# Kernel optimization log

Measured on AMD Instinct MI355X. Metric: run time of the kernel, lower is better.

Reference implementation:

```python
import jax, jax.numpy as jnp
from jax import lax
import numpy as np

SOBEL_X = jnp.array([[-1., 0., 1.], [-2., 0., 2.], [-1., 0., 1.]], dtype=jnp.float32)
SOBEL_Y = jnp.array([[-1., -2., -1.], [0., 0., 0.], [1., 2., 1.]], dtype=jnp.float32)
ALIVE_CH = 3
ALIVE_TH = 0.1
DROPOUT = 0.0
CLAMP = 5.0


def _dwconv3(x, k):
    """Depthwise 3x3 conv, padding=1 (SAME). x: [B,C,H,W], k: [3,3]."""
    C = x.shape[1]
    kern = jnp.tile(k[None, None], (C, 1, 1, 1))  # [C,1,3,3] OIHW, groups=C
    return lax.conv_general_dilated(
        x, kern, window_strides=(1, 1), padding='SAME',
        feature_group_count=C, dimension_numbers=('NCHW', 'OIHW', 'NCHW'))


def _maxpool3(a):
    """3x3 max pool, stride 1, padding 1. a: [B,1,H,W]."""
    return lax.reduce_window(a, -jnp.inf, lax.max, (1, 1, 3, 3), (1, 1, 1, 1), 'SAME')


def setup_inputs() -> dict:
    key = jax.random.key(0)
    kx, k1, k2 = jax.random.split(key, 3)
    B, C, H, W = 8, 16, 128, 128
    hidden = 128
    x = jax.random.uniform(kx, (B, C, H, W), dtype=jnp.float32)  # alive-ish states
    w1 = jax.random.normal(k1, (hidden, 3 * C), dtype=jnp.float32) * 0.05
    b1 = jnp.zeros((hidden,), dtype=jnp.float32)
    w2 = jax.random.normal(k2, (C, hidden), dtype=jnp.float32) * 0.05
    b2 = jnp.zeros((C,), dtype=jnp.float32)
    return {"x": x, "w1": w1, "b1": b1, "w2": w2, "b2": b2, "num_steps": 8}


def reference(x, w1, b1, w2, b2, num_steps):
    keys = jax.random.split(jax.random.key(42), num_steps)

    def step(s, k):
        # pre-update alive mask: maxpool over alive channel > threshold
        pre = _maxpool3(s[:, ALIVE_CH:ALIVE_CH + 1]) > ALIVE_TH  # [B,1,H,W] bool
        # stochastic update mask (dropout=0 -> effectively all ones)
        upd_mask = (jax.random.uniform(k, s.shape) > DROPOUT).astype(s.dtype)
        # perceive: identity conv (padding=1) == s itself; sobel depthwise convs
        perceived = jnp.concatenate(
            [s, _dwconv3(s, SOBEL_X), _dwconv3(s, SOBEL_Y)], axis=1)  # [B,3C,H,W]
        # pointwise update MLP (1x1 convs)
        h = jax.nn.relu(jnp.einsum('bchw,oc->bohw', perceived, w1)
                        + b1[None, :, None, None])
        dx = jnp.einsum('bchw,oc->bohw', h, w2) + b2[None, :, None, None]
        # residual update with clamp
        dx = jnp.clip(dx, -CLAMP, CLAMP)
        s = s + upd_mask * dx
        # post-update alive mask; keep cells alive both before and after
        post = _maxpool3(s[:, ALIVE_CH:ALIVE_CH + 1]) > ALIVE_TH
        s = s * (pre & post).astype(s.dtype)
        return s, None

    x, _ = lax.scan(step, x, keys)
    return x
```

## Files before the change

### kernel.cpp

```cpp
#include <hip/hip_runtime.h>
#include <stdint.h>


#define BATCH 8
#define CH 16
#define HT 128
#define WD 128
#define HIDN 128
#define PLANE (HT*WD)
#define IMG (CH*PLANE)
#define NELEM (BATCH*IMG)
#define NPIX (BATCH*PLANE)
#define WORDS_PER_STEP (NELEM/32)
#define NSTEPS 8

#define PSTR 72
#define PLO_OFF 2304
#define KCM_OFF 4608
#define KF_OFF  5056
#define WREG    5504

typedef _Float16 f16x8 __attribute__((ext_vector_type(8)));
typedef _Float16 f16x4 __attribute__((ext_vector_type(4)));
typedef float    f32x4 __attribute__((ext_vector_type(4)));

struct Keys { unsigned k[2*NSTEPS]; };

__host__ __device__ __forceinline__ unsigned rotl32u(unsigned v, int r) {
  return (v << r) | (v >> (32 - r));
}

__host__ __device__ __forceinline__ void tf2x32(unsigned k0, unsigned k1,
                                                unsigned c0, unsigned c1,
                                                unsigned &o0, unsigned &o1) {
  const unsigned ks2 = k0 ^ k1 ^ 0x1BD11BDAu;
  unsigned x0 = c0 + k0, x1 = c1 + k1;
  x0 += x1; x1 = rotl32u(x1, 13); x1 ^= x0;
  x0 += x1; x1 = rotl32u(x1, 15); x1 ^= x0;
  x0 += x1; x1 = rotl32u(x1, 26); x1 ^= x0;
  x0 += x1; x1 = rotl32u(x1,  6); x1 ^= x0;
  x0 += k1; x1 += ks2 + 1u;
  x0 += x1; x1 = rotl32u(x1, 17); x1 ^= x0;
  x0 += x1; x1 = rotl32u(x1, 29); x1 ^= x0;
  x0 += x1; x1 = rotl32u(x1, 16); x1 ^= x0;
  x0 += x1; x1 = rotl32u(x1, 24); x1 ^= x0;
  x0 += ks2; x1 += k0 + 2u;
  x0 += x1; x1 = rotl32u(x1, 13); x1 ^= x0;
  x0 += x1; x1 = rotl32u(x1, 15); x1 ^= x0;
  x0 += x1; x1 = rotl32u(x1, 26); x1 ^= x0;
  x0 += x1; x1 = rotl32u(x1,  6); x1 ^= x0;
  x0 += k0; x1 += k1 + 3u;
  x0 += x1; x1 = rotl32u(x1, 17); x1 ^= x0;
  x0 += x1; x1 = rotl32u(x1, 29); x1 ^= x0;
  x0 += x1; x1 = rotl32u(x1, 16); x1 ^= x0;
  x0 += x1; x1 = rotl32u(x1, 24); x1 ^= x0;
  x0 += k1; x1 += ks2 + 4u;
  x0 += x1; x1 = rotl32u(x1, 13); x1 ^= x0;
  x0 += x1; x1 = rotl32u(x1, 15); x1 ^= x0;
  x0 += x1; x1 = rotl32u(x1, 26); x1 ^= x0;
  x0 += x1; x1 = rotl32u(x1,  6); x1 ^= x0;
  x0 += ks2; x1 += k0 + 5u;
  o0 = x0; o1 = x1;
}

__global__ __launch_bounds__(256) void mask_kernel(unsigned* __restrict__ mask,
                                                   Keys keys) {
  unsigned t = blockIdx.x * 256u + threadIdx.x;
  unsigned step = t >> 16;
  unsigned k0 = keys.k[2*step], k1 = keys.k[2*step + 1];
  unsigned base = (t & 65535u) << 5;
  unsigned word = 0u;
  #pragma unroll 4
  for (int i = 0; i < 32; ++i) {
    unsigned b1x, b2x;
    tf2x32(k0, k1, 0u, base + (unsigned)i, b1x, b2x);
    unsigned bits = b1x ^ b2x;
    word |= (((bits >> 9) != 0u) ? 1u : 0u) << i;
  }
  mask[t] = word;
}

__global__ __launch_bounds__(256) void wpack_kernel(
    const float* __restrict__ w1, const float* __restrict__ w2,
    _Float16* __restrict__ w1fh, _Float16* __restrict__ w1fl,
    _Float16* __restrict__ w2fh, _Float16* __restrict__ w2fl) {
  int t = blockIdx.x * 256 + threadIdx.x;
  if (t < 8192) {
    int lane = (t >> 3) & 63, i = t & 7;
    int kt = t >> 12, nt = (t >> 9) & 7;
    int k = kt * 32 + (lane >> 4) * 8 + i;
    int n = nt * 16 + (lane & 15);
    float v = (k < 48) ? w1[n * 48 + k] : 0.f;
    _Float16 h = (_Float16)v;
    w1fh[t] = h;
    w1fl[t] = (_Float16)(v - (float)h);
  } else {
    int u = t - 8192;
    int lane = (u >> 3) & 63, i = u & 7;
    int kt = u >> 9;
    int g = (lane >> 4) & 3;
    int o = lane & 15;
    int kk = (i < 4) ? (4 * g + i) : (16 + 4 * g + (i - 4));
    float v = w2[o * HIDN + kt * 32 + kk];
    _Float16 h = (_Float16)v;
    w2fh[u] = h;
    w2fl[u] = (_Float16)(v - (float)h);
  }
}

__global__ __launch_bounds__(256, 3) void step_mfma(
    const float* __restrict__ s,
    const f16x8* __restrict__ w1fh, const f16x8* __restrict__ w1fl,
    const f16x8* __restrict__ w2fh, const f16x8* __restrict__ w2fl,
    const float* __restrict__ bias1, const float* __restrict__ bias2,
    const unsigned* __restrict__ mask,
    float* __restrict__ mid,
    const float* __restrict__ mid3cR,
    float* __restrict__ mid3cW,
    const unsigned char* __restrict__ preR,
    unsigned char* __restrict__ preW,
    const int hasKill) {
  __shared__ __align__(16) char smem[4 * WREG];
  const int tid = threadIdx.x;
  const int wv = tid >> 6;
  const int l  = tid & 63;
  const int p  = l & 15;
  const int g  = l >> 4;
  char* wb = smem + wv * WREG;
  _Float16* Phi = (_Float16*)wb;
  _Float16* Plo = (_Float16*)(wb + PLO_OFF);
  float*    kcm = (float*)(wb + KCM_OFF);
  float*    kfl = (float*)(wb + KF_OFF);

  const int pid0 = blockIdx.x * 128 + wv * 32;
  const int b  = pid0 >> 14;
  const int r0 = pid0 & 16383;
  const int y  = r0 >> 7;
  const int x0 = r0 & 127;
  const bool yu = (y > 0), yd = (y < HT - 1);

  if (hasKill) {
    const float* m3 = mid3cR + b * PLANE;
    #pragma unroll
    for (int rr = 0; rr < 2; ++rr) {
      const int e = l + rr * 64;
      if (e < 108) {
        const int kr = e / 36;
        const int kc = e - kr * 36;
        const int xx = x0 - 2 + kc;
        float cm = -1e30f;
        if ((unsigned)xx < WD) {
          #pragma unroll
          for (int dr = -1; dr <= 1; ++dr) {
            const int ry = y - 1 + kr + dr;
            if ((unsigned)ry < HT) cm = fmaxf(cm, m3[ry * WD + xx]);
          }
        }
        kcm[kr * 36 + kc] = cm;
      }
    }
    asm volatile("" ::: "memory");
    const unsigned char* prb = preR + b * PLANE;
    #pragma unroll
    for (int rr = 0; rr < 2; ++rr) {
      const int e = l + rr * 64;
      if (e < 102) {
        const int kr = e / 34;
        const int kc = e - kr * 34;
        const int yy = y - 1 + kr;
        const int xx = x0 - 1 + kc;
        float kf = 0.f;
        if ((unsigned)yy < HT && (unsigned)xx < WD) {
          const float* c0 = kcm + kr * 36 + kc;
          float mx = fmaxf(fmaxf(c0[0], c0[1]), c0[2]);
          kf = ((mx > 0.1f) && prb[yy * WD + xx]) ? 1.f : 0.f;
        }
        kfl[kr * 36 + kc] = kf;
      }
    }
  } else {
    #pragma unroll
    for (int rr = 0; rr < 2; ++rr) {
      const int e = l + rr * 64;
      if (e < 108) kfl[e] = 1.f;
    }
  }

  const float4 b2q = *(const float4*)(bias2 + g * 4);
  unsigned mw[4];
  #pragma unroll
  for (int cc = 0; cc < 4; ++cc)
    mw[cc] = mask[((b * CH + g * 4 + cc) * HT + y) * (WD / 32) + (x0 >> 5)];

  {
    uint4 z; z.x = 0u; z.y = 0u; z.z = 0u; z.w = 0u;
    _Float16* zb = (l & 32) ? Plo : Phi;
    *(uint4*)(zb + (l & 15) * PSTR + 48 + ((l >> 4) & 1) * 8) = z;
  }

  asm volatile("" ::: "memory");

  const float* sb = s + b * IMG;
  float sctr[2][4];
  float premax[2] = {-1e30f, -1e30f};
  f16x8 pbh[2][2], pbl[2][2];
  #pragma unroll
  for (int t = 0; t < 2; ++t) {
    const int xt = x0 + 16 * t + p;
    const int ctr = y * WD + xt;
    const bool xl = (xt > 0), xr = (xt < WD - 1);
    float kf9[9];
    {
      const int kc = 16 * t + p;
      #pragma unroll
      for (int dy2 = 0; dy2 < 3; ++dy2)
        #pragma unroll
        for (int dx2 = 0; dx2 < 3; ++dx2)
          kf9[dy2 * 3 + dx2] = kfl[dy2 * 36 + kc + dx2];
    }
    f16x4 vh0, vh1, vh2, vl0, vl1, vl2;
    #pragma unroll
    for (int cc = 0; cc < 4; ++cc) {
      const int c = g * 4 + cc;
      const float* sc = sb + c * PLANE + ctr;
      float a11 = sc[0] * kf9[4];
      float a00 = ((yu && xl) ? sc[-WD - 1] : 0.f) * kf9[0];
      float a01 = (yu         ? sc[-WD]     : 0.f) * kf9[1];
      float a02 = ((yu && xr) ? sc[-WD + 1] : 0.f) * kf9[2];
      float a10 = (xl         ? sc[-1]      : 0.f) * kf9[3];
      float a12 = (xr         ? sc[1]       : 0.f) * kf9[5];
      float a20 = ((yd && xl) ? sc[WD - 1]  : 0.f) * kf9[6];
      float a21 = (yd         ? sc[WD]      : 0.f) * kf9[7];
      float a22 = ((yd && xr) ? sc[WD + 1]  : 0.f) * kf9[8];
      float sx = (a02 - a00) + 2.f * (a12 - a10) + (a22 - a20);
      float sy = (a20 - a00) + 2.f * (a21 - a01) + (a22 - a02);
      sctr[t][cc] = a11;
      _Float16 h0 = (_Float16)a11;
      _Float16 h1 = (_Float16)sx;
      _Float16 h2 = (_Float16)sy;
      vh0[cc] = h0; vl0[cc] = (_Float16)(a11 - (float)h0);
      vh1[cc] = h1; vl1[cc] = (_Float16)(sx - (float)h1);
      vh2[cc] = h2; vl2[cc] = (_Float16)(sy - (float)h2);
      if (g == 0 && cc == 3) {
        float m0 = fmaxf(fmaxf(a00, a01), fmaxf(a02, a10));
        float m1 = fmaxf(fmaxf(a11, a12), fmaxf(a20, a21));
        premax[t] = fmaxf(fmaxf(m0, m1), a22);
      }
    }
    *(f16x4*)(Phi + p * PSTR + 4 * g)      = vh0;
    *(f16x4*)(Phi + p * PSTR + 16 + 4 * g) = vh1;
    *(f16x4*)(Phi + p * PSTR + 32 + 4 * g) = vh2;
    *(f16x4*)(Plo + p * PSTR + 4 * g)      = vl0;
    *(f16x4*)(Plo + p * PSTR + 16 + 4 * g) = vl1;
    *(f16x4*)(Plo + p * PSTR + 32 + 4 * g) = vl2;
    asm volatile("" ::: "memory");
    const _Float16* prow = Phi + p * PSTR;
    const _Float16* lrow = Plo + p * PSTR;
    pbh[t][0] = *(const f16x8*)(prow + g * 8);
    pbh[t][1] = *(const f16x8*)(prow + 32 + g * 8);
    pbl[t][0] = *(const f16x8*)(lrow + g * 8);
    pbl[t][1] = *(const f16x8*)(lrow + 32 + g * 8);
    asm volatile("" ::: "memory");
  }

  f32x4 acc[2][8];
  #pragma unroll
  for (int nt = 0; nt < 8; ++nt) {
    const float4 bq = *(const float4*)(bias1 + nt * 16 + 4 * g);
    f32x4 v = {bq.x, bq.y, bq.z, bq.w};
    acc[0][nt] = v;
    acc[1][nt] = v;
  }
  #pragma unroll
  for (int nt = 0; nt < 8; ++nt) {
    f16x8 w1h0 = w1fh[nt * 64 + l];
    f16x8 w1h1 = w1fh[512 + nt * 64 + l];
    f16x8 w1l0 = w1fl[nt * 64 + l];
    f16x8 w1l1 = w1fl[512 + nt * 64 + l];
    #pragma unroll
    for (int t = 0; t < 2; ++t) {
      acc[t][nt] = __builtin_amdgcn_mfma_f32_16x16x32_f16(w1h0, pbh[t][0], acc[t][nt], 0, 0, 0);
      acc[t][nt] = __builtin_amdgcn_mfma_f32_16x16x32_f16(w1h1, pbh[t][1], acc[t][nt], 0, 0, 0);
      acc[t][nt] = __builtin_amdgcn_mfma_f32_16x16x32_f16(w1l0, pbh[t][0], acc[t][nt], 0, 0, 0);
      acc[t][nt] = __builtin_amdgcn_mfma_f32_16x16x32_f16(w1l1, pbh[t][1], acc[t][nt], 0, 0, 0);
      acc[t][nt] = __builtin_amdgcn_mfma_f32_16x16x32_f16(w1h0, pbl[t][0], acc[t][nt], 0, 0, 0);
      acc[t][nt] = __builtin_amdgcn_mfma_f32_16x16x32_f16(w1h1, pbl[t][1], acc[t][nt], 0, 0, 0);
    }
  }

  f16x8 w2h[4], w2l[4];
  #pragma unroll
  for (int kt = 0; kt < 4; ++kt) {
    w2h[kt] = w2fh[kt * 64 + l];
    w2l[kt] = w2fl[kt * 64 + l];
  }

  f32x4 dxr[2];
  #pragma unroll
  for (int t = 0; t < 2; ++t) {
    f16x8 hB[4], lB[4];
    #pragma unroll
    for (int kt = 0; kt < 4; ++kt) {
      #pragma unroll
      for (int i2 = 0; i2 < 4; ++i2) {
        float h0 = fmaxf(acc[t][2 * kt][i2], 0.f);
        _Float16 hh0 = (_Float16)h0;
        hB[kt][i2] = hh0;
        lB[kt][i2] = (_Float16)(h0 - (float)hh0);
        float h1 = fmaxf(acc[t][2 * kt + 1][i2], 0.f);
        _Float16 hh1 = (_Float16)h1;
        hB[kt][4 + i2] = hh1;
        lB[kt][4 + i2] = (_Float16)(h1 - (float)hh1);
      }
    }
    f32x4 accP = {b2q.x, b2q.y, b2q.z, b2q.w};
    f32x4 accQ = {0.f, 0.f, 0.f, 0.f};
    f32x4 accR = {0.f, 0.f, 0.f, 0.f};
    #pragma unroll
    for (int kt = 0; kt < 4; ++kt) {
      accP = __builtin_amdgcn_mfma_f32_16x16x32_f16(w2h[kt], hB[kt], accP, 0, 0, 0);
      accQ = __builtin_amdgcn_mfma_f32_16x16x32_f16(w2l[kt], hB[kt], accQ, 0, 0, 0);
      accR = __builtin_amdgcn_mfma_f32_16x16x32_f16(w2h[kt], lB[kt], accR, 0, 0, 0);
    }
    dxr[t] = (accP + accQ) + accR;
  }

  if (g == 0) {
    preW[pid0 + p]      = (premax[0] > 0.1f) ? 1 : 0;
    preW[pid0 + 16 + p] = (premax[1] > 0.1f) ? 1 : 0;
  }

  #pragma unroll
  for (int t = 0; t < 2; ++t) {
    const int xt = x0 + 16 * t + p;
    const int rt = y * WD + xt;
    #pragma unroll
    for (int cc = 0; cc < 4; ++cc) {
      const int c = g * 4 + cc;
      float d = dxr[t][cc];
      d = fminf(fmaxf(d, -5.f), 5.f);
      float v = sctr[t][cc] + (((mw[cc] >> (16 * t + p)) & 1u) ? d : 0.f);
      mid[b * IMG + c * PLANE + rt] = v;
      if (g == 0 && cc == 3) mid3cW[pid0 + 16 * t + p] = v;
    }
  }
}

__global__ __launch_bounds__(256) void step_b(
    const float* __restrict__ mid,
    const unsigned char* __restrict__ pre,
    float* __restrict__ out) {
  int t = blockIdx.x * 256 + threadIdx.x;
  int cq = t >> 15;
  int qid = t & 32767;
  int b = qid >> 12;
  int r = qid & 4095;
  int y = r >> 5;
  int x0 = (r & 31) * 4;
  const float* m3 = mid + b * IMG + 3 * PLANE;

  float col[6];
  #pragma unroll
  for (int j = 0; j < 6; ++j) {
    int xx = x0 - 1 + j;
    float m = -1e30f;
    if ((unsigned)xx < WD) {
      #pragma unroll
      for (int dy = -1; dy <= 1; ++dy) {
        int yy = y + dy;
        if ((unsigned)yy < HT) m = fmaxf(m, m3[yy * WD + xx]);
      }
    }
    col[j] = m;
  }

  const unsigned char* pr = pre + b * PLANE + y * WD + x0;
  float f[4];
  #pragma unroll
  for (int i = 0; i < 4; ++i) {
    float mx = fmaxf(fmaxf(col[i], col[i + 1]), col[i + 2]);
    f[i] = ((mx > 0.1f) && pr[i]) ? 1.f : 0.f;
  }

  #pragma unroll
  for (int cc = 0; cc < 4; ++cc) {
    int c = cq * 4 + cc;
    const float4 v = *(const float4*)&mid[b * IMG + c * PLANE + y * WD + x0];
    float4 w;
    w.x = v.x * f[0]; w.y = v.y * f[1]; w.z = v.z * f[2]; w.w = v.w * f[3];
    *(float4*)&out[b * IMG + c * PLANE + y * WD + x0] = w;
  }
}

extern "C" void kernel_launch(void* const* d_in, const int* in_sizes, int n_in,
                              void* d_out, int out_size, void* d_ws, size_t ws_size,
                              hipStream_t stream) {
  const float* x  = (const float*)d_in[0];
  const float* w1 = (const float*)d_in[1];
  const float* b1 = (const float*)d_in[2];
  const float* w2 = (const float*)d_in[3];
  const float* b2 = (const float*)d_in[4];
  float* out = (float*)d_out;

  char* ws = (char*)d_ws;
  float* midbuf[2];
  midbuf[0] = (float*)ws;
  midbuf[1] = (float*)(ws + (size_t)NELEM * 4);
  float* m3b[2];
  m3b[0] = (float*)(ws + 2 * (size_t)NELEM * 4);
  m3b[1] = m3b[0] + NPIX;
  unsigned char* preb[2];
  preb[0] = (unsigned char*)(ws + 2 * (size_t)NELEM * 4 + 2 * (size_t)NPIX * 4);
  preb[1] = preb[0] + NPIX;
  unsigned* mask = (unsigned*)(ws + 2 * (size_t)NELEM * 4
                                  + 2 * (size_t)NPIX * 4 + 2 * (size_t)NPIX);
  _Float16* w1fh = (_Float16*)((char*)mask
                               + (size_t)NSTEPS * WORDS_PER_STEP * 4);
  _Float16* w1fl = w1fh + 8192;
  _Float16* w2fh = w1fl + 8192;
  _Float16* w2fl = w2fh + 2048;

  Keys keys;
  for (int j = 0; j < NSTEPS; ++j) {
    unsigned a, b;
    tf2x32(0u, 42u, 0u, (unsigned)j, a, b);
    keys.k[2 * j] = a; keys.k[2 * j + 1] = b;
  }

  mask_kernel<<<(NSTEPS * WORDS_PER_STEP) / 256, 256, 0, stream>>>(mask, keys);
  wpack_kernel<<<40, 256, 0, stream>>>(w1, w2, w1fh, w1fl, w2fh, w2fl);

  for (int s = 0; s < NSTEPS; ++s) {
    const float* src = (s == 0) ? x : midbuf[(s - 1) & 1];
    const int cur = s & 1, prv = cur ^ 1;
    step_mfma<<<NPIX / 128, 256, 0, stream>>>(
        src,
        (const f16x8*)w1fh, (const f16x8*)w1fl,
        (const f16x8*)w2fh, (const f16x8*)w2fl,
        b1, b2, mask + s * WORDS_PER_STEP,
        midbuf[cur],
        m3b[prv], m3b[cur],
        preb[prv], preb[cur],
        (s > 0) ? 1 : 0);
  }
  step_b<<<NPIX / 256, 256, 0, stream>>>(
      midbuf[(NSTEPS - 1) & 1], preb[(NSTEPS - 1) & 1], out);
}
```

Before: 266.8 us.

## Fuse threefry dropout mask generation into step kernel and prefetch stencil taps

Removes the separate mask_kernel, which precomputed dropout bitmasks for all steps, and instead generates each wave's mask words inside step_mfma with threefry, passing the per-step keys as kernel arguments and combining bytes via lane shuffles into shared memory. The 9-tap stencil loads are also hoisted to the start of the kernel, ahead of the alive-mask computation, so global loads overlap with the mask and kill setup. This drops one launch and the mask memory traffic, but adds threefry ALU work and register pressure (72 tap floats per thread) to the main step kernel.

```diff
diff --git a/kernel.cpp b/kernel.cpp
--- a/kernel.cpp
+++ b/kernel.cpp
@@ -11,14 +11,14 @@
 #define IMG (CH*PLANE)
 #define NELEM (BATCH*IMG)
 #define NPIX (BATCH*PLANE)
-#define WORDS_PER_STEP (NELEM/32)
 #define NSTEPS 8
 
 #define PSTR 72
 #define PLO_OFF 2304
 #define KCM_OFF 4608
 #define KF_OFF  5056
-#define WREG    5504
+#define KMW_OFF 5488
+#define WREG    5552
 
 typedef _Float16 f16x8 __attribute__((ext_vector_type(8)));
 typedef _Float16 f16x4 __attribute__((ext_vector_type(4)));
@@ -63,23 +63,6 @@
   o0 = x0; o1 = x1;
 }
 
-__global__ __launch_bounds__(256) void mask_kernel(unsigned* __restrict__ mask,
-                                                   Keys keys) {
-  unsigned t = blockIdx.x * 256u + threadIdx.x;
-  unsigned step = t >> 16;
-  unsigned k0 = keys.k[2*step], k1 = keys.k[2*step + 1];
-  unsigned base = (t & 65535u) << 5;
-  unsigned word = 0u;
-  #pragma unroll 4
-  for (int i = 0; i < 32; ++i) {
-    unsigned b1x, b2x;
-    tf2x32(k0, k1, 0u, base + (unsigned)i, b1x, b2x);
-    unsigned bits = b1x ^ b2x;
-    word |= (((bits >> 9) != 0u) ? 1u : 0u) << i;
-  }
-  mask[t] = word;
-}
-
 __global__ __launch_bounds__(256) void wpack_kernel(
     const float* __restrict__ w1, const float* __restrict__ w2,
     _Float16* __restrict__ w1fh, _Float16* __restrict__ w1fl,
@@ -113,12 +96,12 @@
     const f16x8* __restrict__ w1fh, const f16x8* __restrict__ w1fl,
     const f16x8* __restrict__ w2fh, const f16x8* __restrict__ w2fl,
     const float* __restrict__ bias1, const float* __restrict__ bias2,
-    const unsigned* __restrict__ mask,
     float* __restrict__ mid,
     const float* __restrict__ mid3cR,
     float* __restrict__ mid3cW,
     const unsigned char* __restrict__ preR,
     unsigned char* __restrict__ preW,
+    const unsigned k0s, const unsigned k1s,
     const int hasKill) {
   __shared__ __align__(16) char smem[4 * WREG];
   const int tid = threadIdx.x;
@@ -131,6 +114,7 @@
   _Float16* Plo = (_Float16*)(wb + PLO_OFF);
   float*    kcm = (float*)(wb + KCM_OFF);
   float*    kfl = (float*)(wb + KF_OFF);
+  unsigned* kmw = (unsigned*)(wb + KMW_OFF);
 
   const int pid0 = blockIdx.x * 128 + wv * 32;
   const int b  = pid0 >> 14;
@@ -138,6 +122,28 @@
   const int y  = r0 >> 7;
   const int x0 = r0 & 127;
   const bool yu = (y > 0), yd = (y < HT - 1);
+
+  const float* sb = s + b * IMG;
+  float tap[2][4][9];
+  #pragma unroll
+  for (int t = 0; t < 2; ++t) {
+    const int xt = x0 + 16 * t + p;
+    const int ctr = y * WD + xt;
+    const bool xl = (xt > 0), xr = (xt < WD - 1);
+    #pragma unroll
+    for (int cc = 0; cc < 4; ++cc) {
+      const float* sc = sb + (g * 4 + cc) * PLANE + ctr;
+      tap[t][cc][4] = sc[0];
+      tap[t][cc][0] = (yu && xl) ? sc[-WD - 1] : 0.f;
+      tap[t][cc][1] = yu         ? sc[-WD]     : 0.f;
+      tap[t][cc][2] = (yu && xr) ? sc[-WD + 1] : 0.f;
+      tap[t][cc][3] = xl         ? sc[-1]      : 0.f;
+      tap[t][cc][5] = xr         ? sc[1]       : 0.f;
+      tap[t][cc][6] = (yd && xl) ? sc[WD - 1]  : 0.f;
+      tap[t][cc][7] = yd         ? sc[WD]      : 0.f;
+      tap[t][cc][8] = (yd && xr) ? sc[WD + 1]  : 0.f;
+    }
+  }
 
   if (hasKill) {
     const float* m3 = mid3cR + b * PLANE;
@@ -159,6 +165,29 @@
         kcm[kr * 36 + kc] = cm;
       }
     }
+  }
+
+  {
+    const int c16 = l >> 2;
+    const int q   = l & 3;
+    const unsigned widx = (((unsigned)(b * CH + c16) * HT + (unsigned)y) << 2)
+                          + (unsigned)(x0 >> 5);
+    const unsigned ebase = (widx << 5) + (unsigned)(q * 8);
+    unsigned byte = 0u;
+    #pragma unroll
+    for (int j = 0; j < 8; ++j) {
+      unsigned o0, o1;
+      tf2x32(k0s, k1s, 0u, ebase + (unsigned)j, o0, o1);
+      unsigned bits = o0 ^ o1;
+      byte |= (((bits >> 9) != 0u) ? 1u : 0u) << j;
+    }
+    unsigned part = byte << (q * 8);
+    part |= (unsigned)__shfl_xor((int)part, 1);
+    part |= (unsigned)__shfl_xor((int)part, 2);
+    if (q == 0) kmw[c16] = part;
+  }
+
+  if (hasKill) {
     asm volatile("" ::: "memory");
     const unsigned char* prb = preR + b * PLANE;
     #pragma unroll
@@ -187,11 +216,6 @@
   }
 
   const float4 b2q = *(const float4*)(bias2 + g * 4);
-  unsigned mw[4];
-  #pragma unroll
-  for (int cc = 0; cc < 4; ++cc)
-    mw[cc] = mask[((b * CH + g * 4 + cc) * HT + y) * (WD / 32) + (x0 >> 5)];
-
   {
     uint4 z; z.x = 0u; z.y = 0u; z.z = 0u; z.w = 0u;
     _Float16* zb = (l & 32) ? Plo : Phi;
@@ -200,15 +224,15 @@
 
   asm volatile("" ::: "memory");
 
-  const float* sb = s + b * IMG;
+  unsigned mw[4];
+  #pragma unroll
+  for (int cc = 0; cc < 4; ++cc) mw[cc] = kmw[g * 4 + cc];
+
   float sctr[2][4];
   float premax[2] = {-1e30f, -1e30f};
   f16x8 pbh[2][2], pbl[2][2];
   #pragma unroll
   for (int t = 0; t < 2; ++t) {
-    const int xt = x0 + 16 * t + p;
-    const int ctr = y * WD + xt;
-    const bool xl = (xt > 0), xr = (xt < WD - 1);
     float kf9[9];
     {
       const int kc = 16 * t + p;
@@ -221,17 +245,15 @@
     f16x4 vh0, vh1, vh2, vl0, vl1, vl2;
     #pragma unroll
     for (int cc = 0; cc < 4; ++cc) {
-      const int c = g * 4 + cc;
-      const float* sc = sb + c * PLANE + ctr;
-      float a11 = sc[0] * kf9[4];
-      float a00 = ((yu && xl) ? sc[-WD - 1] : 0.f) * kf9[0];
-      float a01 = (yu         ? sc[-WD]     : 0.f) * kf9[1];
-      float a02 = ((yu && xr) ? sc[-WD + 1] : 0.f) * kf9[2];
-      float a10 = (xl         ? sc[-1]      : 0.f) * kf9[3];
-      float a12 = (xr         ? sc[1]       : 0.f) * kf9[5];
-      float a20 = ((yd && xl) ? sc[WD - 1]  : 0.f) * kf9[6];
-      float a21 = (yd         ? sc[WD]      : 0.f) * kf9[7];
-      float a22 = ((yd && xr) ? sc[WD + 1]  : 0.f) * kf9[8];
+      float a11 = tap[t][cc][4] * kf9[4];
+      float a00 = tap[t][cc][0] * kf9[0];
+      float a01 = tap[t][cc][1] * kf9[1];
+      float a02 = tap[t][cc][2] * kf9[2];
+      float a10 = tap[t][cc][3] * kf9[3];
+      float a12 = tap[t][cc][5] * kf9[5];
+      float a20 = tap[t][cc][6] * kf9[6];
+      float a21 = tap[t][cc][7] * kf9[7];
+      float a22 = tap[t][cc][8] * kf9[8];
       float sx = (a02 - a00) + 2.f * (a12 - a10) + (a22 - a20);
       float sy = (a20 - a00) + 2.f * (a21 - a01) + (a22 - a02);
       sctr[t][cc] = a11;
@@ -412,10 +434,8 @@
   unsigned char* preb[2];
   preb[0] = (unsigned char*)(ws + 2 * (size_t)NELEM * 4 + 2 * (size_t)NPIX * 4);
   preb[1] = preb[0] + NPIX;
-  unsigned* mask = (unsigned*)(ws + 2 * (size_t)NELEM * 4
-                                  + 2 * (size_t)NPIX * 4 + 2 * (size_t)NPIX);
-  _Float16* w1fh = (_Float16*)((char*)mask
-                               + (size_t)NSTEPS * WORDS_PER_STEP * 4);
+  _Float16* w1fh = (_Float16*)(ws + 2 * (size_t)NELEM * 4
+                               + 2 * (size_t)NPIX * 4 + 2 * (size_t)NPIX);
   _Float16* w1fl = w1fh + 8192;
   _Float16* w2fh = w1fl + 8192;
   _Float16* w2fl = w2fh + 2048;
@@ -427,7 +447,6 @@
     keys.k[2 * j] = a; keys.k[2 * j + 1] = b;
   }
 
-  mask_kernel<<<(NSTEPS * WORDS_PER_STEP) / 256, 256, 0, stream>>>(mask, keys);
   wpack_kernel<<<40, 256, 0, stream>>>(w1, w2, w1fh, w1fl, w2fh, w2fl);
 
   for (int s = 0; s < NSTEPS; ++s) {
@@ -437,10 +456,11 @@
         src,
         (const f16x8*)w1fh, (const f16x8*)w1fl,
         (const f16x8*)w2fh, (const f16x8*)w2fl,
-        b1, b2, mask + s * WORDS_PER_STEP,
+        b1, b2,
         midbuf[cur],
         m3b[prv], m3b[cur],
         preb[prv], preb[cur],
+        keys.k[2 * s], keys.k[2 * s + 1],
         (s > 0) ? 1 : 0);
   }
   step_b<<<NPIX / 256, 256, 0, stream>>>(
```

Result: slower. 274.2 us (+2.8%).

## Fold per-step RNG mask generation into step kernels as extra blocks

Applied to the files above, without the earlier changes.

Removes the standalone mask_kernel that generated all eight steps' dropout masks up front. Step 0's mask is now generated by extra blocks appended to the weight-pack launch, and each step kernel appends extra blocks that generate the next step's mask. The Threefry work then overlaps with the memory-bound step work instead of running serially. The cost is more blocks per step launch, and mask blocks may take CU slots from step blocks in the tail.

```diff
diff --git a/kernel.cpp b/kernel.cpp
--- a/kernel.cpp
+++ b/kernel.cpp
@@ -13,12 +13,16 @@
 #define NPIX (BATCH*PLANE)
 #define WORDS_PER_STEP (NELEM/32)
 #define NSTEPS 8
+#define STEP_BLOCKS (NPIX/128)
+#define MASK_BLOCKS (WORDS_PER_STEP/256)
 
 #define PSTR 72
 #define PLO_OFF 2304
 #define KCM_OFF 4608
 #define KF_OFF  5056
 #define WREG    5504
+
+#define MEM_FENCE() asm volatile("" ::: "memory")
 
 typedef _Float16 f16x8 __attribute__((ext_vector_type(8)));
 typedef _Float16 f16x4 __attribute__((ext_vector_type(4)));
@@ -63,12 +67,9 @@
   o0 = x0; o1 = x1;
 }
 
-__global__ __launch_bounds__(256) void mask_kernel(unsigned* __restrict__ mask,
-                                                   Keys keys) {
-  unsigned t = blockIdx.x * 256u + threadIdx.x;
-  unsigned step = t >> 16;
-  unsigned k0 = keys.k[2*step], k1 = keys.k[2*step + 1];
-  unsigned base = (t & 65535u) << 5;
+__device__ __forceinline__ unsigned mask_word(unsigned k0, unsigned k1,
+                                              unsigned wid) {
+  const unsigned base = wid << 5;
   unsigned word = 0u;
   #pragma unroll 4
   for (int i = 0; i < 32; ++i) {
@@ -77,13 +78,19 @@
     unsigned bits = b1x ^ b2x;
     word |= (((bits >> 9) != 0u) ? 1u : 0u) << i;
   }
-  mask[t] = word;
+  return word;
 }
 
 __global__ __launch_bounds__(256) void wpack_kernel(
     const float* __restrict__ w1, const float* __restrict__ w2,
     _Float16* __restrict__ w1fh, _Float16* __restrict__ w1fl,
-    _Float16* __restrict__ w2fh, _Float16* __restrict__ w2fl) {
+    _Float16* __restrict__ w2fh, _Float16* __restrict__ w2fl,
+    unsigned* __restrict__ mask0, unsigned mk0, unsigned mk1) {
+  if (blockIdx.x >= 40) {
+    const unsigned wid = (blockIdx.x - 40) * 256u + threadIdx.x;
+    mask0[wid] = mask_word(mk0, mk1, wid);
+    return;
+  }
   int t = blockIdx.x * 256 + threadIdx.x;
   if (t < 8192) {
     int lane = (t >> 3) & 63, i = t & 7;
@@ -114,12 +121,20 @@
     const f16x8* __restrict__ w2fh, const f16x8* __restrict__ w2fl,
     const float* __restrict__ bias1, const float* __restrict__ bias2,
     const unsigned* __restrict__ mask,
+    unsigned* __restrict__ maskN,
+    const unsigned kn0, const unsigned kn1,
     float* __restrict__ mid,
     const float* __restrict__ mid3cR,
     float* __restrict__ mid3cW,
     const unsigned char* __restrict__ preR,
     unsigned char* __restrict__ preW,
     const int hasKill) {
+  if (blockIdx.x >= STEP_BLOCKS) {
+    const unsigned wid = (blockIdx.x - STEP_BLOCKS) * 256u + threadIdx.x;
+    maskN[wid] = mask_word(kn0, kn1, wid);
+    return;
+  }
+
   __shared__ __align__(16) char smem[4 * WREG];
   const int tid = threadIdx.x;
   const int wv = tid >> 6;
@@ -159,7 +174,7 @@
         kcm[kr * 36 + kc] = cm;
       }
     }
-    asm volatile("" ::: "memory");
+    MEM_FENCE();
     const unsigned char* prb = preR + b * PLANE;
     #pragma unroll
     for (int rr = 0; rr < 2; ++rr) {
@@ -198,7 +213,7 @@
     *(uint4*)(zb + (l & 15) * PSTR + 48 + ((l >> 4) & 1) * 8) = z;
   }
 
-  asm volatile("" ::: "memory");
+  MEM_FENCE();
 
   const float* sb = s + b * IMG;
   float sctr[2][4];
@@ -253,14 +268,14 @@
     *(f16x4*)(Plo + p * PSTR + 4 * g)      = vl0;
     *(f16x4*)(Plo + p * PSTR + 16 + 4 * g) = vl1;
     *(f16x4*)(Plo + p * PSTR + 32 + 4 * g) = vl2;
-    asm volatile("" ::: "memory");
+    MEM_FENCE();
     const _Float16* prow = Phi + p * PSTR;
     const _Float16* lrow = Plo + p * PSTR;
     pbh[t][0] = *(const f16x8*)(prow + g * 8);
     pbh[t][1] = *(const f16x8*)(prow + 32 + g * 8);
     pbl[t][0] = *(const f16x8*)(lrow + g * 8);
     pbl[t][1] = *(const f16x8*)(lrow + 32 + g * 8);
-    asm volatile("" ::: "memory");
+    MEM_FENCE();
   }
 
   f32x4 acc[2][8];
@@ -427,17 +442,22 @@
     keys.k[2 * j] = a; keys.k[2 * j + 1] = b;
   }
 
-  mask_kernel<<<(NSTEPS * WORDS_PER_STEP) / 256, 256, 0, stream>>>(mask, keys);
-  wpack_kernel<<<40, 256, 0, stream>>>(w1, w2, w1fh, w1fl, w2fh, w2fl);
+  wpack_kernel<<<40 + MASK_BLOCKS, 256, 0, stream>>>(
+      w1, w2, w1fh, w1fl, w2fh, w2fl, mask, keys.k[0], keys.k[1]);
 
   for (int s = 0; s < NSTEPS; ++s) {
     const float* src = (s == 0) ? x : midbuf[(s - 1) & 1];
     const int cur = s & 1, prv = cur ^ 1;
-    step_mfma<<<NPIX / 128, 256, 0, stream>>>(
+    const bool genNext = (s + 1 < NSTEPS);
+    step_mfma<<<STEP_BLOCKS + (genNext ? MASK_BLOCKS : 0), 256, 0, stream>>>(
         src,
         (const f16x8*)w1fh, (const f16x8*)w1fl,
         (const f16x8*)w2fh, (const f16x8*)w2fl,
-        b1, b2, mask + s * WORDS_PER_STEP,
+        b1, b2,
+        mask + s * WORDS_PER_STEP,
+        mask + (genNext ? (s + 1) : s) * WORDS_PER_STEP,
+        keys.k[2 * (genNext ? (s + 1) : s)],
+        keys.k[2 * (genNext ? (s + 1) : s) + 1],
         midbuf[cur],
         m3b[prv], m3b[cur],
         preb[prv], preb[cur],
```

Result: faster. 247.0 us (-7.4%).
